# Performance work log

Hardware: AMD Instinct MI355X
Metric: run time of the kernel (lower is better)

The kernel has to match this reference:

```python
import jax, jax.numpy as jnp
from jax import lax
import numpy as np

# Mamba mixer dims (mamba-1.4b scale)
D_MODEL, D_INNER, D_STATE, D_CONV, DT_RANK = 2048, 4096, 16, 4, 128
B, L = 2, 1024


def setup_inputs() -> dict:
    key = jax.random.key(0)
    ks = jax.random.split(key, 10)
    s = 0.02
    x = jax.random.normal(ks[0], (B, L, D_MODEL), jnp.float32)
    W_in = jax.random.normal(ks[1], (2 * D_INNER, D_MODEL), jnp.float32) * s
    conv_w = jax.random.normal(ks[2], (D_INNER, D_CONV), jnp.float32) * s  # depthwise kernel
    conv_b = jax.random.normal(ks[3], (D_INNER,), jnp.float32) * s
    W_x = jax.random.normal(ks[4], (DT_RANK + 2 * D_STATE, D_INNER), jnp.float32) * s
    W_dt = jax.random.normal(ks[5], (D_INNER, DT_RANK), jnp.float32) * s
    b_dt = jax.random.normal(ks[6], (D_INNER,), jnp.float32) * s
    # S4D-real init: A = -[1..d_state] per channel
    A_log = jnp.log(jnp.broadcast_to(jnp.arange(1, D_STATE + 1, dtype=jnp.float32), (D_INNER, D_STATE)))
    Dp = jnp.ones((D_INNER,), jnp.float32)
    W_out = jax.random.normal(ks[7], (D_MODEL, D_INNER), jnp.float32) * s
    return {"x": x, "W_in": W_in, "conv_w": conv_w, "conv_b": conv_b,
            "W_x": W_x, "W_dt": W_dt, "b_dt": b_dt, "A_log": A_log,
            "Dp": Dp, "W_out": W_out}


def reference(x, W_in, conv_w, conv_b, W_x, W_dt, b_dt, A_log, Dp, W_out):
    b, l, _ = x.shape
    d_inner, d_state = A_log.shape
    dt_rank = W_dt.shape[1]
    d_conv = conv_w.shape[1]

    # in_proj -> x branch and gate z   [b,l,2*d_inner]
    xz = jnp.einsum('bld,ed->ble', x, W_in)
    xp, z = jnp.split(xz, 2, axis=-1)

    # causal depthwise conv1d (kernel size d_conv) + SiLU
    xpad = jnp.pad(xp, ((0, 0), (d_conv - 1, 0), (0, 0)))
    xc = conv_b + sum(xpad[:, k:k + l, :] * conv_w[:, k] for k in range(d_conv))
    xc = jax.nn.silu(xc)

    # input-dependent dt, B, C
    dbc = jnp.einsum('ble,fe->blf', xc, W_x)
    dt = dbc[..., :dt_rank]
    Bm = dbc[..., dt_rank:dt_rank + d_state]          # [b,l,s]
    Cm = dbc[..., dt_rank + d_state:]                 # [b,l,s]
    delta = jax.nn.softplus(jnp.einsum('blr,er->ble', dt, W_dt) + b_dt)  # [b,l,e]

    A = -jnp.exp(A_log)                               # [e,s]
    dA = jnp.exp(delta[..., None] * A)                # [b,l,e,s]
    dBx = delta[..., None] * Bm[:, :, None, :] * xc[..., None]  # [b,l,e,s]

    def step(h, inp):
        dA_t, dBx_t = inp                             # [b,e,s]
        h = dA_t * h + dBx_t
        return h, h

    h0 = jnp.zeros((b, d_inner, d_state), x.dtype)
    _, hs = lax.scan(step, h0, (jnp.swapaxes(dA, 0, 1), jnp.swapaxes(dBx, 0, 1)))
    hs = jnp.swapaxes(hs, 0, 1)                       # [b,l,e,s]

    y = jnp.einsum('bles,bls->ble', hs, Cm) + xc * Dp
    y = y * jax.nn.silu(z)
    return jnp.einsum('ble,de->bld', y, W_out)
```

## Files before the change

### kernel.cpp

```cpp
#include <hip/hip_runtime.h>
#include <cstdint>


typedef __bf16 bf16x8 __attribute__((ext_vector_type(8)));
typedef float f32x4 __attribute__((ext_vector_type(4)));

__device__ __forceinline__ unsigned short f2bf(float f) {
  uint32_t u = __float_as_uint(f);
  u += 0x7FFFu + ((u >> 16) & 1u);
  return (unsigned short)(u >> 16);
}

__device__ __forceinline__ float silu_f(float v) {
  return v / (1.f + __expf(-v));
}

__device__ __forceinline__ float softplus_f(float v) {
  return (v > 20.f) ? v : log1pf(__expf(v));
}

__global__ void cast_f32_to_bf16(const float* __restrict__ src,
                                 unsigned short* __restrict__ dst, int n4) {
  int i = blockIdx.x * 256 + threadIdx.x;
  if (i >= n4) return;
  float4 v = reinterpret_cast<const float4*>(src)[i];
  ushort4 o;
  o.x = f2bf(v.x); o.y = f2bf(v.y); o.z = f2bf(v.z); o.w = f2bf(v.w);
  reinterpret_cast<ushort4*>(dst)[i] = o;
}

__global__ void cast_wx_pad(const float* __restrict__ Wx,
                            unsigned short* __restrict__ dst) {
  int i = blockIdx.x * 256 + threadIdx.x;
  int r = i >> 12;
  float v = (r < 160) ? Wx[(size_t)r * 4096 + (i & 4095)] : 0.f;
  dst[i] = f2bf(v);
}

#define BM 128
#define BN 128
#define BKK 32

__device__ __forceinline__ void stage_tile(const unsigned short* __restrict__ G,
                                           int ldK, int g0, int k0,
                                           unsigned short* lds, int wave, int lane) {
#pragma unroll
  for (int c = 0; c < 2; ++c) {
    int row = c * 64 + wave * 16 + (lane >> 2);
    int col = (lane & 3) * 8;
    const unsigned short* src = G + (size_t)(g0 + row) * ldK + (k0 + col);
    unsigned short* dst = lds + c * 2048 + wave * 512;
    __builtin_amdgcn_global_load_lds((__attribute__((address_space(1))) void*)(src),
                                     (__attribute__((address_space(3))) void*)(dst),
                                     16, 0, 0);
  }
}

__global__ __launch_bounds__(256)
void gemm_bt(const unsigned short* __restrict__ A, const unsigned short* __restrict__ B,
             float* __restrict__ C, int M, int N, int ldK, int kchunk,
             const float* __restrict__ bias_sp) {
  __shared__ unsigned short As[BM * BKK];
  __shared__ unsigned short Bs[BN * BKK];
  const int tid = threadIdx.x;
  const int wave = tid >> 6, lane = tid & 63;
  const int wr = wave >> 1, wc = wave & 1;
  const int m0 = blockIdx.y * BM, n0 = blockIdx.x * BN;
  const int lr = lane & 15, lg = lane >> 4;
  const int kb = blockIdx.z * kchunk, ke = kb + kchunk;
  C += (size_t)blockIdx.z * M * N;

  f32x4 zero = {0.f, 0.f, 0.f, 0.f};
  f32x4 acc[4][4];
#pragma unroll
  for (int i = 0; i < 4; ++i)
#pragma unroll
    for (int j = 0; j < 4; ++j) acc[i][j] = zero;

  for (int k0 = kb; k0 < ke; k0 += BKK) {
    stage_tile(A, ldK, m0, k0, As, wave, lane);
    stage_tile(B, ldK, n0, k0, Bs, wave, lane);
    __syncthreads();
    bf16x8 af[4], bfr[4];
#pragma unroll
    for (int i = 0; i < 4; ++i)
      af[i] = *reinterpret_cast<const bf16x8*>(&As[(wr * 64 + i * 16 + lr) * BKK + lg * 8]);
#pragma unroll
    for (int j = 0; j < 4; ++j)
      bfr[j] = *reinterpret_cast<const bf16x8*>(&Bs[(wc * 64 + j * 16 + lr) * BKK + lg * 8]);
#pragma unroll
    for (int i = 0; i < 4; ++i)
#pragma unroll
      for (int j = 0; j < 4; ++j)
        acc[i][j] = __builtin_amdgcn_mfma_f32_16x16x32_bf16(af[i], bfr[j], acc[i][j], 0, 0, 0);
    __syncthreads();
  }

#pragma unroll
  for (int i = 0; i < 4; ++i) {
#pragma unroll
    for (int j = 0; j < 4; ++j) {
      int mrow = m0 + wr * 64 + i * 16 + lg * 4;
      int ncol = n0 + wc * 64 + j * 16 + lr;
      if (bias_sp) {
        float bv = bias_sp[ncol];
#pragma unroll
        for (int r = 0; r < 4; ++r)
          C[(size_t)(mrow + r) * N + ncol] = softplus_f(acc[i][j][r] + bv);
      } else {
#pragma unroll
        for (int r = 0; r < 4; ++r)
          C[(size_t)(mrow + r) * N + ncol] = acc[i][j][r];
      }
    }
  }
}

__global__ void reduce8_dbc(const float* __restrict__ p, float* __restrict__ dbc,
                            unsigned short* __restrict__ dt_bf) {
  int i = blockIdx.x * 256 + threadIdx.x;
  float s = 0.f;
#pragma unroll
  for (int c = 0; c < 8; ++c) s += p[(size_t)c * 524288 + i];
  dbc[i] = s;
  int col = i & 255;
  if (col < 128) dt_bf[(size_t)(i >> 8) * 128 + col] = f2bf(s);
}

__global__ void reduce2_out(const float* __restrict__ p, float* __restrict__ out) {
  int i = blockIdx.x * 256 + threadIdx.x;
  const float4* p4 = reinterpret_cast<const float4*>(p);
  float4 a = p4[i], b = p4[i + 1048576];
  float4 r; r.x = a.x + b.x; r.y = a.y + b.y; r.z = a.z + b.z; r.w = a.w + b.w;
  reinterpret_cast<float4*>(out)[i] = r;
}

__global__ __launch_bounds__(512, 2)
void gemm_bt_8ph(const unsigned short* __restrict__ A,
                 const unsigned short* __restrict__ B,
                 float* __restrict__ C, int M, int N, int K, int nbm) {
  __shared__ unsigned short As[2][16384];
  __shared__ unsigned short Bs[2][16384];
  const int tid = threadIdx.x;
  const int wid = tid >> 6, lane = tid & 63;
  const int wr = wid >> 2, wc = wid & 3;
  const int lr = lane & 15, lg = lane >> 4;

  const int cpx = gridDim.x >> 3;
  const int x = blockIdx.x;
  const int wg = (x & 7) * cpx + (x >> 3);
  const int bm = wg % nbm, bn = wg / nbm;
  const int m0 = bm * 256, n0 = bn * 256;

  f32x4 acc[8][4];
  f32x4 zero = {0.f, 0.f, 0.f, 0.f};
#pragma unroll
  for (int i = 0; i < 8; ++i)
#pragma unroll
    for (int j = 0; j < 4; ++j) acc[i][j] = zero;

  const int nt = K / 64;

  auto QUANT = [&](int t, int q) {
    const int buf = t & 1;
    const int ks = q >> 1;
    const unsigned short* G = (q & 1) ? B : A;
    const int g0 = (q & 1) ? n0 : m0;
    unsigned short* lds = ((q & 1) ? &Bs[buf][0] : &As[buf][0]) + ks * 8192;
    const int k0 = t * 64 + ks * 32;
#pragma unroll
    for (int r = 0; r < 2; ++r) {
      int row = r * 128 + (tid >> 2);
      int scol = ((tid & 3) * 8) ^ (((row >> 1) & 3) << 3);
      const unsigned short* src = G + (size_t)(g0 + row) * K + (k0 + scol);
      __builtin_amdgcn_global_load_lds(
          (__attribute__((address_space(1))) const void*)(src),
          (__attribute__((address_space(3))) void*)(lds + r * 4096 + tid * 8),
          16, 0, 0);
    }
  };

  auto RD_A = [&](int buf, int ks, int mf) -> bf16x8 {
    int row = wr * 128 + mf * 16 + lr;
    int col = (lg * 8) ^ (((row >> 1) & 3) << 3);
    return *reinterpret_cast<const bf16x8*>(&As[buf][ks * 8192 + row * 32 + col]);
  };
  auto RD_B = [&](int buf, int ks, int nf) -> bf16x8 {
    int row = wc * 64 + nf * 16 + lr;
    int col = (lg * 8) ^ (((row >> 1) & 3) << 3);
    return *reinterpret_cast<const bf16x8*>(&Bs[buf][ks * 8192 + row * 32 + col]);
  };

  QUANT(0, 0); QUANT(0, 1); QUANT(0, 2); QUANT(0, 3);
  asm volatile("s_waitcnt vmcnt(4)" ::: "memory");
  __builtin_amdgcn_s_barrier();

  bf16x8 a[8], b[4];
  for (int t = 0; t < nt; ++t) {
    const int buf = t & 1;
    const bool pf = (t + 1 < nt);
#pragma unroll
    for (int mf = 0; mf < 8; ++mf) a[mf] = RD_A(buf, 0, mf);
    b[0] = RD_B(buf, 0, 0); b[1] = RD_B(buf, 0, 1);
    if (pf) {
      QUANT(t + 1, 0);
      asm volatile("s_waitcnt vmcnt(6)" ::: "memory");
    } else {
      asm volatile("s_waitcnt vmcnt(4)" ::: "memory");
    }
    __builtin_amdgcn_s_barrier();
    asm volatile("s_waitcnt lgkmcnt(0)" ::: "memory");
    __builtin_amdgcn_sched_barrier(0);
    __builtin_amdgcn_s_setprio(1);
#pragma unroll
    for (int nf = 0; nf < 2; ++nf)
#pragma unroll
      for (int mf = 0; mf < 8; ++mf)
        acc[mf][nf] = __builtin_amdgcn_mfma_f32_16x16x32_bf16(a[mf], b[nf], acc[mf][nf], 0, 0, 0);
    __builtin_amdgcn_s_setprio(0);
    __builtin_amdgcn_s_barrier();
    b[2] = RD_B(buf, 0, 2); b[3] = RD_B(buf, 0, 3);
    if (pf) {
      QUANT(t + 1, 1);
      asm volatile("s_waitcnt vmcnt(4)" ::: "memory");
    } else {
      asm volatile("s_waitcnt vmcnt(0)" ::: "memory");
    }
    __builtin_amdgcn_s_barrier();
    asm volatile("s_waitcnt lgkmcnt(0)" ::: "memory");
    __builtin_amdgcn_sched_barrier(0);
    __builtin_amdgcn_s_setprio(1);
#pragma unroll
    for (int nf = 2; nf < 4; ++nf)
#pragma unroll
      for (int mf = 0; mf < 8; ++mf)
        acc[mf][nf] = __builtin_amdgcn_mfma_f32_16x16x32_bf16(a[mf], b[nf], acc[mf][nf], 0, 0, 0);
    __builtin_amdgcn_s_setprio(0);
    __builtin_amdgcn_s_barrier();
#pragma unroll
    for (int mf = 0; mf < 8; ++mf) a[mf] = RD_A(buf, 1, mf);
    b[0] = RD_B(buf, 1, 0); b[1] = RD_B(buf, 1, 1);
    if (pf) QUANT(t + 1, 2);
    __builtin_amdgcn_s_barrier();
    asm volatile("s_waitcnt lgkmcnt(0)" ::: "memory");
    __builtin_amdgcn_sched_barrier(0);
    __builtin_amdgcn_s_setprio(1);
#pragma unroll
    for (int nf = 0; nf < 2; ++nf)
#pragma unroll
      for (int mf = 0; mf < 8; ++mf)
        acc[mf][nf] = __builtin_amdgcn_mfma_f32_16x16x32_bf16(a[mf], b[nf], acc[mf][nf], 0, 0, 0);
    __builtin_amdgcn_s_setprio(0);
    __builtin_amdgcn_s_barrier();
    b[2] = RD_B(buf, 1, 2); b[3] = RD_B(buf, 1, 3);
    if (pf) {
      QUANT(t + 1, 3);
      asm volatile("s_waitcnt vmcnt(4)" ::: "memory");
    }
    __builtin_amdgcn_s_barrier();
    asm volatile("s_waitcnt lgkmcnt(0)" ::: "memory");
    __builtin_amdgcn_sched_barrier(0);
    __builtin_amdgcn_s_setprio(1);
#pragma unroll
    for (int nf = 2; nf < 4; ++nf)
#pragma unroll
      for (int mf = 0; mf < 8; ++mf)
        acc[mf][nf] = __builtin_amdgcn_mfma_f32_16x16x32_bf16(a[mf], b[nf], acc[mf][nf], 0, 0, 0);
    __builtin_amdgcn_s_setprio(0);
    __builtin_amdgcn_s_barrier();
  }

#pragma unroll
  for (int mf = 0; mf < 8; ++mf) {
#pragma unroll
    for (int nf = 0; nf < 4; ++nf) {
      int mrow = m0 + wr * 128 + mf * 16 + lg * 4;
      int ncol = n0 + wc * 64 + nf * 16 + lr;
#pragma unroll
      for (int r = 0; r < 4; ++r)
        C[(size_t)(mrow + r) * N + ncol] = acc[mf][nf][r];
    }
  }
}

__global__ void conv_silu_kernel(const float* __restrict__ xz,
                                 const float* __restrict__ conv_w,
                                 const float* __restrict__ conv_b,
                                 float* __restrict__ xc,
                                 unsigned short* __restrict__ xc_bf) {
  int i4 = blockIdx.x * 256 + threadIdx.x;
  int e4 = i4 & 1023;
  int m = i4 >> 10;
  int l = m & 1023;
  float4 cw0 = reinterpret_cast<const float4*>(conv_w)[e4 * 4 + 0];
  float4 cw1 = reinterpret_cast<const float4*>(conv_w)[e4 * 4 + 1];
  float4 cw2 = reinterpret_cast<const float4*>(conv_w)[e4 * 4 + 2];
  float4 cw3 = reinterpret_cast<const float4*>(conv_w)[e4 * 4 + 3];
  float4 acc = reinterpret_cast<const float4*>(conv_b)[e4];
#pragma unroll
  for (int k = 0; k < 4; ++k) {
    if (l - 3 + k >= 0) {
      float4 xv = reinterpret_cast<const float4*>(xz)[(size_t)(m - 3 + k) * 2048 + e4];
      acc.x = fmaf(xv.x, ((const float*)&cw0)[k], acc.x);
      acc.y = fmaf(xv.y, ((const float*)&cw1)[k], acc.y);
      acc.z = fmaf(xv.z, ((const float*)&cw2)[k], acc.z);
      acc.w = fmaf(xv.w, ((const float*)&cw3)[k], acc.w);
    }
  }
  float4 s;
  s.x = silu_f(acc.x); s.y = silu_f(acc.y);
  s.z = silu_f(acc.z); s.w = silu_f(acc.w);
  reinterpret_cast<float4*>(xc)[i4] = s;
  ushort4 o;
  o.x = f2bf(s.x); o.y = f2bf(s.y); o.z = f2bf(s.z); o.w = f2bf(s.w);
  reinterpret_cast<ushort4*>(xc_bf)[i4] = o;
}

__global__ __launch_bounds__(256)
void scan_pass1(const float* __restrict__ delta, const float* __restrict__ dbc,
                const float* __restrict__ xc, const float* __restrict__ A_log,
                float* __restrict__ hfin, float* __restrict__ Pprod) {
  __shared__ float Bsh[1024];
  const int tid = threadIdx.x;
  const int bc = blockIdx.x >> 4;
  const int eg = blockIdx.x & 15;
  const int b = bc >> 4, c = bc & 15;
  const int e = eg * 256 + tid;
  const int mb = b * 1024 + c * 64;
  for (int i = tid; i < 1024; i += 256)
    Bsh[i] = dbc[(size_t)(mb + (i >> 4)) * 256 + 128 + (i & 15)];
  __syncthreads();

  float A[16];
  const float4* al = reinterpret_cast<const float4*>(A_log + (size_t)e * 16);
#pragma unroll
  for (int q = 0; q < 4; ++q) {
    float4 v = al[q];
    A[q * 4 + 0] = -__expf(v.x); A[q * 4 + 1] = -__expf(v.y);
    A[q * 4 + 2] = -__expf(v.z); A[q * 4 + 3] = -__expf(v.w);
  }
  float h[16], P[16];
#pragma unroll
  for (int s = 0; s < 16; ++s) { h[s] = 0.f; P[s] = 1.f; }

  for (int ll = 0; ll < 64; ++ll) {
    const size_t m = (size_t)(mb + ll);
    float dl = delta[m * 4096 + e];
    float dxc = dl * xc[m * 4096 + e];
#pragma unroll
    for (int s = 0; s < 16; ++s) {
      float dA = __expf(dl * A[s]);
      P[s] *= dA;
      h[s] = fmaf(dA, h[s], Bsh[ll * 16 + s] * dxc);
    }
  }
  float* hp = hfin + ((size_t)bc * 4096 + e) * 16;
  float* pp = Pprod + ((size_t)bc * 4096 + e) * 16;
#pragma unroll
  for (int s = 0; s < 16; ++s) { hp[s] = h[s]; pp[s] = P[s]; }
}

__global__ void scan_pass2(float* __restrict__ hfin, const float* __restrict__ Pprod) {
  int idx = blockIdx.x * 256 + threadIdx.x;
  int b = idx >> 16;
  int es = idx & 65535;
  float H = 0.f;
  for (int c = 0; c < 16; ++c) {
    size_t o = ((size_t)(b * 16 + c) << 16) + es;
    float hf = hfin[o];
    float Pp = Pprod[o];
    hfin[o] = H;
    H = fmaf(Pp, H, hf);
  }
}

__global__ __launch_bounds__(256)
void scan_pass3(const float* __restrict__ delta, const float* __restrict__ dbc,
                const float* __restrict__ xc, const float* __restrict__ xz,
                const float* __restrict__ A_log, const float* __restrict__ Dp,
                const float* __restrict__ hcarry, unsigned short* __restrict__ y_bf) {
  __shared__ float Bsh[1024];
  __shared__ float Csh[1024];
  const int tid = threadIdx.x;
  const int bc = blockIdx.x >> 4;
  const int eg = blockIdx.x & 15;
  const int b = bc >> 4, c = bc & 15;
  const int e = eg * 256 + tid;
  const int mb = b * 1024 + c * 64;
  for (int i = tid; i < 1024; i += 256) {
    size_t base = (size_t)(mb + (i >> 4)) * 256 + (i & 15);
    Bsh[i] = dbc[base + 128];
    Csh[i] = dbc[base + 144];
  }
  __syncthreads();

  float A[16];
  const float4* al = reinterpret_cast<const float4*>(A_log + (size_t)e * 16);
#pragma unroll
  for (int q = 0; q < 4; ++q) {
    float4 v = al[q];
    A[q * 4 + 0] = -__expf(v.x); A[q * 4 + 1] = -__expf(v.y);
    A[q * 4 + 2] = -__expf(v.z); A[q * 4 + 3] = -__expf(v.w);
  }
  float h[16];
  const float* hp = hcarry + ((size_t)bc * 4096 + e) * 16;
#pragma unroll
  for (int s = 0; s < 16; ++s) h[s] = hp[s];
  const float Dv = Dp[e];

  for (int ll = 0; ll < 64; ++ll) {
    const size_t m = (size_t)(mb + ll);
    float dl = delta[m * 4096 + e];
    float xcv = xc[m * 4096 + e];
    float dxc = dl * xcv;
    float y = 0.f;
#pragma unroll
    for (int s = 0; s < 16; ++s) {
      float dA = __expf(dl * A[s]);
      h[s] = fmaf(dA, h[s], Bsh[ll * 16 + s] * dxc);
      y = fmaf(h[s], Csh[ll * 16 + s], y);
    }
    float z = xz[m * 8192 + 4096 + e];
    y = (y + xcv * Dv) * silu_f(z);
    y_bf[m * 4096 + e] = f2bf(y);
  }
}

extern "C" void kernel_launch(void* const* d_in, const int* in_sizes, int n_in,
                              void* d_out, int out_size, void* d_ws, size_t ws_size,
                              hipStream_t stream) {
  const float* x      = (const float*)d_in[0];
  const float* W_in   = (const float*)d_in[1];
  const float* conv_w = (const float*)d_in[2];
  const float* conv_b = (const float*)d_in[3];
  const float* W_x    = (const float*)d_in[4];
  const float* W_dt   = (const float*)d_in[5];
  const float* b_dt   = (const float*)d_in[6];
  const float* A_log  = (const float*)d_in[7];
  const float* Dp     = (const float*)d_in[8];
  const float* W_out  = (const float*)d_in[9];
  float* out = (float*)d_out;
  char* ws = (char*)d_ws;

  unsigned short* Win_bf    = (unsigned short*)(ws + 0);
  float*          gpart     = (float*)(ws + 0);
  float*          delta     = (float*)(ws + 0);
  unsigned short* x_bf      = (unsigned short*)(ws + 33554432);
  unsigned short* y_bf      = (unsigned short*)(ws + 33554432);
  unsigned short* Wout_bf   = (unsigned short*)(ws + 50331648);
  unsigned short* Wx_bf     = (unsigned short*)(ws + 67108864);
  unsigned short* Wdt_bf    = (unsigned short*)(ws + 69206016);
  float*          xz        = (float*)(ws + 70254592);
  float*          xc        = (float*)(ws + 137363456);
  unsigned short* xc_bf     = (unsigned short*)(ws + 170917888);
  float*          hfin      = (float*)(ws + 170917888);
  float*          Pprod     = (float*)(ws + 179306496);
  float*          dbc       = (float*)(ws + 187695104);
  unsigned short* dt_bf     = (unsigned short*)(ws + 189792256);

  cast_f32_to_bf16<<<4096, 256, 0, stream>>>(x, x_bf, 1048576);
  cast_f32_to_bf16<<<16384, 256, 0, stream>>>(W_in, Win_bf, 4194304);
  cast_f32_to_bf16<<<8192, 256, 0, stream>>>(W_out, Wout_bf, 2097152);
  cast_wx_pad<<<4096, 256, 0, stream>>>(W_x, Wx_bf);
  cast_f32_to_bf16<<<512, 256, 0, stream>>>(W_dt, Wdt_bf, 131072);

  gemm_bt_8ph<<<256, 512, 0, stream>>>(x_bf, Win_bf, xz, 2048, 8192, 2048, 8);

  conv_silu_kernel<<<8192, 256, 0, stream>>>(xz, conv_w, conv_b, xc, xc_bf);

  gemm_bt<<<dim3(2, 16, 8), 256, 0, stream>>>(xc_bf, Wx_bf, gpart, 2048, 256, 4096, 512, nullptr);
  reduce8_dbc<<<2048, 256, 0, stream>>>(gpart, dbc, dt_bf);

  gemm_bt<<<dim3(32, 16, 1), 256, 0, stream>>>(dt_bf, Wdt_bf, delta, 2048, 4096, 128, 128, b_dt);

  scan_pass1<<<512, 256, 0, stream>>>(delta, dbc, xc, A_log, hfin, Pprod);
  scan_pass2<<<512, 256, 0, stream>>>(hfin, Pprod);
  scan_pass3<<<512, 256, 0, stream>>>(delta, dbc, xc, xz, A_log, Dp, hfin, y_bf);

  gemm_bt<<<dim3(16, 16, 2), 256, 0, stream>>>(y_bf, Wout_bf, gpart, 2048, 2048, 4096, 2048, nullptr);
  reduce2_out<<<4096, 256, 0, stream>>>(gpart, out);
}
```

Baseline: 366.6 us.

## Fuse weight casts, drop fp32 xc buffer, use 256-tile split-K GEMM for out_proj

Merges the five cast launches into one kernel and stops writing the fp32 xc tensor; the scan kernels now read the bf16 xc copy instead, which cuts memory traffic but lowers the precision of xc in the scan. The out projection moves from the 128-tile gemm_bt with split-K 2 to the 256-tile 8-phase GEMM with split-K 4, which needs a 4-way reduction. Workspace is reshuffled so the split-K partials reuse the xz region after the scan has consumed it.

```diff
diff --git a/kernel.cpp b/kernel.cpp
--- a/kernel.cpp
+++ b/kernel.cpp
@@ -11,6 +11,10 @@
   return (unsigned short)(u >> 16);
 }
 
+__device__ __forceinline__ float bf2f(unsigned short v) {
+  return __uint_as_float(((uint32_t)v) << 16);
+}
+
 __device__ __forceinline__ float silu_f(float v) {
   return v / (1.f + __expf(-v));
 }
@@ -19,22 +23,31 @@
   return (v > 20.f) ? v : log1pf(__expf(v));
 }
 
-__global__ void cast_f32_to_bf16(const float* __restrict__ src,
-                                 unsigned short* __restrict__ dst, int n4) {
+__global__ void cast_all(const float* __restrict__ x, const float* __restrict__ W_in,
+                         const float* __restrict__ W_out, const float* __restrict__ W_dt,
+                         const float* __restrict__ W_x,
+                         unsigned short* __restrict__ x_bf, unsigned short* __restrict__ Win_bf,
+                         unsigned short* __restrict__ Wout_bf, unsigned short* __restrict__ Wdt_bf,
+                         unsigned short* __restrict__ Wx_bf) {
   int i = blockIdx.x * 256 + threadIdx.x;
-  if (i >= n4) return;
-  float4 v = reinterpret_cast<const float4*>(src)[i];
-  ushort4 o;
-  o.x = f2bf(v.x); o.y = f2bf(v.y); o.z = f2bf(v.z); o.w = f2bf(v.w);
-  reinterpret_cast<ushort4*>(dst)[i] = o;
-}
-
-__global__ void cast_wx_pad(const float* __restrict__ Wx,
-                            unsigned short* __restrict__ dst) {
-  int i = blockIdx.x * 256 + threadIdx.x;
-  int r = i >> 12;
-  float v = (r < 160) ? Wx[(size_t)r * 4096 + (i & 4095)] : 0.f;
-  dst[i] = f2bf(v);
+  const float4* s4; ushort4* d4; int j;
+  if (i < 1048576)      { s4 = (const float4*)x;     d4 = (ushort4*)x_bf;    j = i; }
+  else if (i < 5242880) { s4 = (const float4*)W_in;  d4 = (ushort4*)Win_bf;  j = i - 1048576; }
+  else if (i < 7340032) { s4 = (const float4*)W_out; d4 = (ushort4*)Wout_bf; j = i - 5242880; }
+  else if (i < 7471104) { s4 = (const float4*)W_dt;  d4 = (ushort4*)Wdt_bf;  j = i - 7340032; }
+  else {
+    j = i - 7471104;
+    ushort4 o = {0, 0, 0, 0};
+    if (j < 163840) {
+      float4 v = ((const float4*)W_x)[j];
+      o.x = f2bf(v.x); o.y = f2bf(v.y); o.z = f2bf(v.z); o.w = f2bf(v.w);
+    }
+    ((ushort4*)Wx_bf)[j] = o;
+    return;
+  }
+  float4 v = s4[j];
+  ushort4 o; o.x = f2bf(v.x); o.y = f2bf(v.y); o.z = f2bf(v.z); o.w = f2bf(v.w);
+  d4[j] = o;
 }
 
 #define BM 128
@@ -127,18 +140,20 @@
   if (col < 128) dt_bf[(size_t)(i >> 8) * 128 + col] = f2bf(s);
 }
 
-__global__ void reduce2_out(const float* __restrict__ p, float* __restrict__ out) {
+__global__ void reduce4_out(const float* __restrict__ p, float* __restrict__ out) {
   int i = blockIdx.x * 256 + threadIdx.x;
   const float4* p4 = reinterpret_cast<const float4*>(p);
-  float4 a = p4[i], b = p4[i + 1048576];
-  float4 r; r.x = a.x + b.x; r.y = a.y + b.y; r.z = a.z + b.z; r.w = a.w + b.w;
+  float4 a = p4[i], b = p4[i + 1048576], c = p4[i + 2097152], d = p4[i + 3145728];
+  float4 r;
+  r.x = (a.x + b.x) + (c.x + d.x); r.y = (a.y + b.y) + (c.y + d.y);
+  r.z = (a.z + b.z) + (c.z + d.z); r.w = (a.w + b.w) + (c.w + d.w);
   reinterpret_cast<float4*>(out)[i] = r;
 }
 
 __global__ __launch_bounds__(512, 2)
 void gemm_bt_8ph(const unsigned short* __restrict__ A,
                  const unsigned short* __restrict__ B,
-                 float* __restrict__ C, int M, int N, int K, int nbm) {
+                 float* __restrict__ C, int M, int N, int K, int nbm, int kchunk) {
   __shared__ unsigned short As[2][16384];
   __shared__ unsigned short Bs[2][16384];
   const int tid = threadIdx.x;
@@ -151,6 +166,8 @@
   const int wg = (x & 7) * cpx + (x >> 3);
   const int bm = wg % nbm, bn = wg / nbm;
   const int m0 = bm * 256, n0 = bn * 256;
+  const int kb = blockIdx.z * kchunk;
+  C += (size_t)blockIdx.z * M * N;
 
   f32x4 acc[8][4];
   f32x4 zero = {0.f, 0.f, 0.f, 0.f};
@@ -159,7 +176,7 @@
 #pragma unroll
     for (int j = 0; j < 4; ++j) acc[i][j] = zero;
 
-  const int nt = K / 64;
+  const int nt = kchunk / 64;
 
   auto QUANT = [&](int t, int q) {
     const int buf = t & 1;
@@ -167,7 +184,7 @@
     const unsigned short* G = (q & 1) ? B : A;
     const int g0 = (q & 1) ? n0 : m0;
     unsigned short* lds = ((q & 1) ? &Bs[buf][0] : &As[buf][0]) + ks * 8192;
-    const int k0 = t * 64 + ks * 32;
+    const int k0 = kb + t * 64 + ks * 32;
 #pragma unroll
     for (int r = 0; r < 2; ++r) {
       int row = r * 128 + (tid >> 2);
@@ -286,7 +303,6 @@
 __global__ void conv_silu_kernel(const float* __restrict__ xz,
                                  const float* __restrict__ conv_w,
                                  const float* __restrict__ conv_b,
-                                 float* __restrict__ xc,
                                  unsigned short* __restrict__ xc_bf) {
   int i4 = blockIdx.x * 256 + threadIdx.x;
   int e4 = i4 & 1023;
@@ -307,18 +323,15 @@
       acc.w = fmaf(xv.w, ((const float*)&cw3)[k], acc.w);
     }
   }
-  float4 s;
-  s.x = silu_f(acc.x); s.y = silu_f(acc.y);
-  s.z = silu_f(acc.z); s.w = silu_f(acc.w);
-  reinterpret_cast<float4*>(xc)[i4] = s;
   ushort4 o;
-  o.x = f2bf(s.x); o.y = f2bf(s.y); o.z = f2bf(s.z); o.w = f2bf(s.w);
+  o.x = f2bf(silu_f(acc.x)); o.y = f2bf(silu_f(acc.y));
+  o.z = f2bf(silu_f(acc.z)); o.w = f2bf(silu_f(acc.w));
   reinterpret_cast<ushort4*>(xc_bf)[i4] = o;
 }
 
 __global__ __launch_bounds__(256)
 void scan_pass1(const float* __restrict__ delta, const float* __restrict__ dbc,
-                const float* __restrict__ xc, const float* __restrict__ A_log,
+                const unsigned short* __restrict__ xcb, const float* __restrict__ A_log,
                 float* __restrict__ hfin, float* __restrict__ Pprod) {
   __shared__ float Bsh[1024];
   const int tid = threadIdx.x;
@@ -346,7 +359,7 @@
   for (int ll = 0; ll < 64; ++ll) {
     const size_t m = (size_t)(mb + ll);
     float dl = delta[m * 4096 + e];
-    float dxc = dl * xc[m * 4096 + e];
+    float dxc = dl * bf2f(xcb[m * 4096 + e]);
 #pragma unroll
     for (int s = 0; s < 16; ++s) {
       float dA = __expf(dl * A[s]);
@@ -376,7 +389,7 @@
 
 __global__ __launch_bounds__(256)
 void scan_pass3(const float* __restrict__ delta, const float* __restrict__ dbc,
-                const float* __restrict__ xc, const float* __restrict__ xz,
+                const unsigned short* __restrict__ xcb, const float* __restrict__ xz,
                 const float* __restrict__ A_log, const float* __restrict__ Dp,
                 const float* __restrict__ hcarry, unsigned short* __restrict__ y_bf) {
   __shared__ float Bsh[1024];
@@ -411,7 +424,7 @@
   for (int ll = 0; ll < 64; ++ll) {
     const size_t m = (size_t)(mb + ll);
     float dl = delta[m * 4096 + e];
-    float xcv = xc[m * 4096 + e];
+    float xcv = bf2f(xcb[m * 4096 + e]);
     float dxc = dl * xcv;
     float y = 0.f;
 #pragma unroll
@@ -443,7 +456,7 @@
   char* ws = (char*)d_ws;
 
   unsigned short* Win_bf    = (unsigned short*)(ws + 0);
-  float*          gpart     = (float*)(ws + 0);
+  float*          gpart2    = (float*)(ws + 0);
   float*          delta     = (float*)(ws + 0);
   unsigned short* x_bf      = (unsigned short*)(ws + 33554432);
   unsigned short* y_bf      = (unsigned short*)(ws + 33554432);
@@ -451,32 +464,29 @@
   unsigned short* Wx_bf     = (unsigned short*)(ws + 67108864);
   unsigned short* Wdt_bf    = (unsigned short*)(ws + 69206016);
   float*          xz        = (float*)(ws + 70254592);
-  float*          xc        = (float*)(ws + 137363456);
+  float*          gpart4    = (float*)(ws + 70254592);
   unsigned short* xc_bf     = (unsigned short*)(ws + 170917888);
-  float*          hfin      = (float*)(ws + 170917888);
-  float*          Pprod     = (float*)(ws + 179306496);
+  float*          hfin      = (float*)(ws + 137363456);
+  float*          Pprod     = (float*)(ws + 145752064);
   float*          dbc       = (float*)(ws + 187695104);
   unsigned short* dt_bf     = (unsigned short*)(ws + 189792256);
 
-  cast_f32_to_bf16<<<4096, 256, 0, stream>>>(x, x_bf, 1048576);
-  cast_f32_to_bf16<<<16384, 256, 0, stream>>>(W_in, Win_bf, 4194304);
-  cast_f32_to_bf16<<<8192, 256, 0, stream>>>(W_out, Wout_bf, 2097152);
-  cast_wx_pad<<<4096, 256, 0, stream>>>(W_x, Wx_bf);
-  cast_f32_to_bf16<<<512, 256, 0, stream>>>(W_dt, Wdt_bf, 131072);
-
-  gemm_bt_8ph<<<256, 512, 0, stream>>>(x_bf, Win_bf, xz, 2048, 8192, 2048, 8);
-
-  conv_silu_kernel<<<8192, 256, 0, stream>>>(xz, conv_w, conv_b, xc, xc_bf);
-
-  gemm_bt<<<dim3(2, 16, 8), 256, 0, stream>>>(xc_bf, Wx_bf, gpart, 2048, 256, 4096, 512, nullptr);
-  reduce8_dbc<<<2048, 256, 0, stream>>>(gpart, dbc, dt_bf);
+  cast_all<<<30208, 256, 0, stream>>>(x, W_in, W_out, W_dt, W_x,
+                                      x_bf, Win_bf, Wout_bf, Wdt_bf, Wx_bf);
+
+  gemm_bt_8ph<<<256, 512, 0, stream>>>(x_bf, Win_bf, xz, 2048, 8192, 2048, 8, 2048);
+
+  conv_silu_kernel<<<8192, 256, 0, stream>>>(xz, conv_w, conv_b, xc_bf);
+
+  gemm_bt<<<dim3(2, 16, 8), 256, 0, stream>>>(xc_bf, Wx_bf, gpart2, 2048, 256, 4096, 512, nullptr);
+  reduce8_dbc<<<2048, 256, 0, stream>>>(gpart2, dbc, dt_bf);
 
   gemm_bt<<<dim3(32, 16, 1), 256, 0, stream>>>(dt_bf, Wdt_bf, delta, 2048, 4096, 128, 128, b_dt);
 
-  scan_pass1<<<512, 256, 0, stream>>>(delta, dbc, xc, A_log, hfin, Pprod);
+  scan_pass1<<<512, 256, 0, stream>>>(delta, dbc, xc_bf, A_log, hfin, Pprod);
   scan_pass2<<<512, 256, 0, stream>>>(hfin, Pprod);
-  scan_pass3<<<512, 256, 0, stream>>>(delta, dbc, xc, xz, A_log, Dp, hfin, y_bf);
-
-  gemm_bt<<<dim3(16, 16, 2), 256, 0, stream>>>(y_bf, Wout_bf, gpart, 2048, 2048, 4096, 2048, nullptr);
-  reduce2_out<<<4096, 256, 0, stream>>>(gpart, out);
-}
+  scan_pass3<<<512, 256, 0, stream>>>(delta, dbc, xc_bf, xz, A_log, Dp, hfin, y_bf);
+
+  gemm_bt_8ph<<<dim3(64, 1, 4), 512, 0, stream>>>(y_bf, Wout_bf, gpart4, 2048, 2048, 4096, 8, 1024);
+  reduce4_out<<<4096, 256, 0, stream>>>(gpart4, out);
+}
```

Result: faster. 350.1 us (-4.5%).
